# Optimization experiments

Measured on AMD Instinct MI355X. Metric: run time of the kernel, lower is better.

The kernel has to match this reference:

```python
import jax, jax.numpy as jnp
import numpy as np
from jax import lax

B, FREQ, TIME = 32, 256, 4096   # batch, freq bins, time frames
PAD_LEN = 256                   # cfg['n_peaks']
KSIZE = 5                       # cfg['blur_kernel']
SIGMA = 1.0                     # cfg['blur_sigma']


def setup_inputs() -> dict:
    key = jax.random.key(0)
    return {"spec_tensor": jax.random.normal(key, (B, FREQ, TIME), dtype=jnp.float32)}


def _peak_from_features(f):
    # local maxima along time (1x3) and freq (3x1), SAME padding, stride 1
    neg = jnp.asarray(-jnp.inf, f.dtype)
    max_t = lax.reduce_window(f, neg, lax.max, (1, 1, 3), (1, 1, 1), 'SAME')
    max_f = lax.reduce_window(f, neg, lax.max, (1, 3, 1), (1, 1, 1), 'SAME')
    peaks = ((f == max_t) & (f == max_f)).astype(f.dtype)
    mn = jnp.min(f, axis=(1, 2), keepdims=True)
    mx = jnp.max(f, axis=(1, 2), keepdims=True)
    return peaks * ((f - mn) / (mx - mn))


def _gaussian_blur(x):
    # separable gaussian blur with reflect padding (torchvision semantics)
    half = KSIZE // 2
    coords = jnp.arange(KSIZE, dtype=x.dtype) - half
    g = jnp.exp(-0.5 * (coords / SIGMA) ** 2)
    g = g / jnp.sum(g)
    x4 = jnp.pad(x, ((0, 0), (half, half), (half, half)), mode='reflect')[:, None]  # [B,1,F+2h,T+2h]
    kf = g.reshape(1, 1, KSIZE, 1)
    kt = g.reshape(1, 1, 1, KSIZE)
    y = lax.conv_general_dilated(x4, kf, (1, 1), 'VALID')
    y = lax.conv_general_dilated(y, kt, (1, 1), 'VALID')
    return y[:, 0]


def _extract(flat):
    # compact nonzero entries (row-major order) into fixed PAD_LEN slots, zero padded;
    # entries beyond PAD_LEN are truncated (scatter mode='drop').
    mask = flat > 0
    pos = jnp.cumsum(mask.astype(jnp.int32)) - 1
    dest = jnp.where(mask, pos, PAD_LEN)  # out-of-range -> dropped
    idx = jnp.zeros(PAD_LEN, jnp.int32).at[dest].set(
        jnp.arange(flat.shape[0], dtype=jnp.int32), mode='drop')
    val = jnp.zeros(PAD_LEN, flat.dtype).at[dest].set(flat, mode='drop')
    freq = (idx // TIME).astype(flat.dtype) / FREQ
    time = (idx % TIME).astype(flat.dtype) / TIME
    return jnp.stack([freq, time, val], axis=0)  # [3, PAD_LEN]


def reference(spec_tensor):
    p = _peak_from_features(spec_tensor)
    p = _gaussian_blur(p)
    p = _peak_from_features(p)
    return jax.vmap(_extract)(p.reshape(B, FREQ * TIME))  # [B, 3, PAD_LEN]
```

## Files before the change

kernel.cpp:

```cpp
#include <hip/hip_runtime.h>

#define NB 32
#define NF 256
#define NT 4096
#define PAD_LEN 256

#define TF 16
#define TT 128

#define TS 32
#define NSTRIP (NT / TS)

#define G0 0.054488684f
#define G1 0.24420134f
#define G2 0.40261995f

__device__ __forceinline__ float blur5(float a, float b, float c, float d, float e) {
    return G0 * (a + b) + G1 * (c + d) + G2 * e;
}
__device__ __forceinline__ float4 blur5v(const float4& a, const float4& b, const float4& c,
                                         const float4& d, const float4& e) {
    return make_float4(blur5(a.x, b.x, c.x, d.x, e.x), blur5(a.y, b.y, c.y, d.y, e.y),
                       blur5(a.z, b.z, c.z, d.z, e.z), blur5(a.w, b.w, c.w, d.w, e.w));
}

#define SW 140
#define SW4 35
#define RS 24
#define RP 22
#define RV 18

#define R1_WORDS (RS * SW)
#define R2_WORDS (RP * SW)

__device__ __forceinline__ int reflectF(int i) {
    i = (i < 0) ? -i : i;
    return (i >= NF) ? (2 * NF - 2 - i) : i;
}
__device__ __forceinline__ unsigned encf(float x) {
    unsigned u = __float_as_uint(x);
    return (u & 0x80000000u) ? ~u : (u | 0x80000000u);
}
__device__ __forceinline__ float decf(unsigned e) {
    unsigned u = (e & 0x80000000u) ? (e ^ 0x80000000u) : ~e;
    return __uint_as_float(u);
}

#define MM_OFF 0
#define CNT_OFF 1024
#define PFX_OFF (1024 + NB * NF * 32 * 4)

__global__ __launch_bounds__(256) void k_init(float* __restrict__ out, unsigned* __restrict__ mm,
                                              int* __restrict__ counts2) {
    int tid = blockIdx.x * 256 + threadIdx.x;
    if (tid < NB * 3 * PAD_LEN) out[tid] = 0.0f;
    if (tid < NB) {
        mm[tid * 4 + 0] = 0xFFFFFFFFu;
        mm[tid * 4 + 1] = 0u;
        mm[tid * 4 + 2] = 0xFFFFFFFFu;
        mm[tid * 4 + 3] = 0u;
    }
    for (int i = tid; i < NB * NF * 32; i += 96 * 256) counts2[i] = 0;
}

__global__ __launch_bounds__(256) void k_minmax(const float* __restrict__ spec, unsigned* __restrict__ mm) {
    const int b = blockIdx.y;
    const float4* p = (const float4*)(spec + (size_t)b * NF * NT);
    const int base4 = blockIdx.x * 4096;
    float lmin = __builtin_inff(), lmax = -__builtin_inff();
    for (int i = threadIdx.x; i < 4096; i += 256) {
        float4 v = p[base4 + i];
        lmin = fminf(lmin, fminf(fminf(v.x, v.y), fminf(v.z, v.w)));
        lmax = fmaxf(lmax, fmaxf(fmaxf(v.x, v.y), fmaxf(v.z, v.w)));
    }
    for (int off = 32; off; off >>= 1) {
        lmin = fminf(lmin, __shfl_down(lmin, off));
        lmax = fmaxf(lmax, __shfl_down(lmax, off));
    }
    __shared__ float rmn[4], rmx[4];
    int wave = threadIdx.x >> 6, lane = threadIdx.x & 63;
    if (lane == 0) { rmn[wave] = lmin; rmx[wave] = lmax; }
    __syncthreads();
    if (threadIdx.x == 0) {
        for (int w = 1; w < 4; w++) { lmin = fminf(lmin, rmn[w]); lmax = fmaxf(lmax, rmx[w]); }
        atomicMin(&mm[b * 4 + 0], encf(lmin));
        atomicMax(&mm[b * 4 + 1], encf(lmax));
    }
}


template<int J> __device__ __forceinline__ float getj(const float4& v) {
    if constexpr (J == 0) return v.x;
    else if constexpr (J == 1) return v.y;
    else if constexpr (J == 2) return v.z;
    else return v.w;
}

template<bool DP, bool DH, bool DQ, int J>
__device__ __forceinline__ void march_step(
    const float4& r0, const float4& r1, const float4& r2, const float4& r3,
    float4& Sa, float4& Sb, float4& Sc,
    float4& V0, float4& V1, float4& V2, float4& V3, float4& V4,
    float4& Bm, float4& Bc, float4& Bp,
    int& c0, int& c1, int& c2, int& c3,
    float& lmin, float& lmax,
    const int lane, const int sid, const float mn, const float rinv, const int hb)
{
    const float NEGF = -__builtin_inff();
    float4 X = make_float4(getj<J>(r0), getj<J>(r1), getj<J>(r2), getj<J>(r3));
    Sa = Sb; Sb = Sc; Sc = X;
    if constexpr (DP) {
        float up0 = __shfl_up(Sb.w, 1);
        float dn3 = __shfl_down(Sb.x, 1);
        if (lane == 0)  up0 = NEGF;
        if (lane == 63) dn3 = NEGF;
        float4 P;
        { const float x = Sb.x; const bool pk = (x >= Sa.x) && (x >= Sc.x) && (x >= up0)  && (x >= Sb.y); P.x = pk ? (x - mn) * rinv : 0.0f; }
        { const float x = Sb.y; const bool pk = (x >= Sa.y) && (x >= Sc.y) && (x >= Sb.x) && (x >= Sb.z); P.y = pk ? (x - mn) * rinv : 0.0f; }
        { const float x = Sb.z; const bool pk = (x >= Sa.z) && (x >= Sc.z) && (x >= Sb.y) && (x >= Sb.w); P.z = pk ? (x - mn) * rinv : 0.0f; }
        { const float x = Sb.w; const bool pk = (x >= Sa.w) && (x >= Sc.w) && (x >= Sb.z) && (x >= dn3); P.w = pk ? (x - mn) * rinv : 0.0f; }
        const float pzm = __shfl_up(P.z, 1);
        const float pwm = __shfl_up(P.w, 1);
        const float pxp = __shfl_down(P.x, 1);
        const float pyp = __shfl_down(P.y, 1);
        float4 Vn;
        Vn.x = blur5(pzm, P.z, pwm, P.y, P.x);
        Vn.y = blur5(pwm, P.w, P.x, P.z, P.y);
        Vn.z = blur5(P.x, pxp, P.y, P.w, P.z);
        Vn.w = blur5(P.y, pyp, P.z, pxp, P.w);
        if (lane == 0)  { Vn.x = blur5(P.z, P.z, P.y, P.y, P.x);
                          Vn.y = blur5(P.y, P.w, P.x, P.z, P.y); }
        if (lane == 63) { Vn.z = blur5(P.x, P.z, P.y, P.w, P.z);
                          Vn.w = blur5(P.y, P.y, P.z, P.z, P.w); }
        V0 = V1; V1 = V2; V2 = V3; V3 = V4; V4 = Vn;
    }
    if constexpr (DH) {
        const int h = hb + J;
        float4 Bn;
        if ((unsigned)h < (unsigned)NT) {
            Bn = blur5v(V0, V4, V1, V3, V2);
            if (sid == 0) {
                if (h == 0)      Bn = blur5v(V4, V4, V3, V3, V2);
                else if (h == 1) Bn = blur5v(V2, V4, V1, V3, V2);
            }
            if (sid == NSTRIP - 1) {
                if (h == NT - 2)      Bn = blur5v(V0, V2, V1, V3, V2);
                else if (h == NT - 1) Bn = blur5v(V0, V0, V1, V1, V2);
            }
        } else {
            Bn = make_float4(NEGF, NEGF, NEGF, NEGF);
        }
        Bm = Bc; Bc = Bp; Bp = Bn;
    }
    if constexpr (DQ) {
        float u0 = __shfl_up(Bc.w, 1);
        float d3 = __shfl_down(Bc.x, 1);
        if (lane == 0)  u0 = NEGF;
        if (lane == 63) d3 = NEGF;
        { const float x = Bc.x; const bool pk = (x >= Bm.x) && (x >= Bp.x) && (x >= u0)   && (x >= Bc.y); c0 += (pk && (x > 0.0f)) ? 1 : 0; }
        { const float x = Bc.y; const bool pk = (x >= Bm.y) && (x >= Bp.y) && (x >= Bc.x) && (x >= Bc.z); c1 += (pk && (x > 0.0f)) ? 1 : 0; }
        { const float x = Bc.z; const bool pk = (x >= Bm.z) && (x >= Bp.z) && (x >= Bc.y) && (x >= Bc.w); c2 += (pk && (x > 0.0f)) ? 1 : 0; }
        { const float x = Bc.w; const bool pk = (x >= Bm.w) && (x >= Bp.w) && (x >= Bc.z) && (x >= d3); c3 += (pk && (x > 0.0f)) ? 1 : 0; }
        lmin = fminf(lmin, fminf(fminf(Bc.x, Bc.y), fminf(Bc.z, Bc.w)));
        lmax = fmaxf(lmax, fmaxf(fmaxf(Bc.x, Bc.y), fmaxf(Bc.z, Bc.w)));
    }
}

__global__ __launch_bounds__(256) void k_march(const float* __restrict__ spec,
                                               unsigned* __restrict__ mm,
                                               int* __restrict__ counts2) {
    const int b = blockIdx.y;
    const int lane = threadIdx.x & 63;
    const int wv = threadIdx.x >> 6;
    const int sid = blockIdx.x * 4 + wv;
    const int T0 = sid * TS;

    const float mn = decf(mm[b * 4 + 0]);
    const float mx = decf(mm[b * 4 + 1]);
    const float rinv = 1.0f / (mx - mn);

    const float* base = spec + (size_t)b * NF * NT + (size_t)(4 * lane) * NT;
    const float NEGF = -__builtin_inff();
    const float4 NEG4 = make_float4(NEGF, NEGF, NEGF, NEGF);

    float4 a0, a1, a2, a3, b0, b1, b2, b3;
    float4 Sa = NEG4, Sb = NEG4, Sc = NEG4;
    float4 V0 = NEG4, V1 = NEG4, V2 = NEG4, V3 = NEG4, V4 = NEG4;
    float4 Bm = NEG4, Bc = NEG4, Bp = NEG4;
    int c0 = 0, c1 = 0, c2 = 0, c3 = 0;
    float lmin = __builtin_inff(), lmax = NEGF;

#define LOADG(q0, q1, q2, q3, gg) do {                                     \
    const int tg = T0 - 4 + 4 * (gg);                                      \
    if ((unsigned)tg < (unsigned)NT) {                                     \
        q0 = *(const float4*)(base + tg);                                  \
        q1 = *(const float4*)(base + NT + tg);                             \
        q2 = *(const float4*)(base + 2 * NT + tg);                         \
        q3 = *(const float4*)(base + 3 * NT + tg);                         \
    } else { q0 = NEG4; q1 = NEG4; q2 = NEG4; q3 = NEG4; }                 \
} while (0)

#define MARGS Sa, Sb, Sc, V0, V1, V2, V3, V4, Bm, Bc, Bp, c0, c1, c2, c3, lmin, lmax, lane, sid, mn, rinv

    LOADG(a0, a1, a2, a3, 0);
    LOADG(b0, b1, b2, b3, 1);

    march_step<false, false, false, 0>(a0, a1, a2, a3, MARGS, 0);
    march_step<false, false, false, 1>(a0, a1, a2, a3, MARGS, 0);
    march_step<true,  false, false, 2>(a0, a1, a2, a3, MARGS, 0);
    march_step<true,  false, false, 3>(a0, a1, a2, a3, MARGS, 0);
    LOADG(a0, a1, a2, a3, 2);

    {
        const int hb = T0 - 3;
        march_step<true, false, false, 0>(b0, b1, b2, b3, MARGS, hb);
        march_step<true, false, false, 1>(b0, b1, b2, b3, MARGS, hb);
        march_step<true, true,  false, 2>(b0, b1, b2, b3, MARGS, hb);
        march_step<true, true,  false, 3>(b0, b1, b2, b3, MARGS, hb);
    }
    LOADG(b0, b1, b2, b3, 3);

    for (int g = 2; g <= 8; g += 2) {
        {
            const int hb = T0 - 4 + 4 * g - 3;
            march_step<true, true, true, 0>(a0, a1, a2, a3, MARGS, hb);
            march_step<true, true, true, 1>(a0, a1, a2, a3, MARGS, hb);
            march_step<true, true, true, 2>(a0, a1, a2, a3, MARGS, hb);
            march_step<true, true, true, 3>(a0, a1, a2, a3, MARGS, hb);
        }
        if (g + 2 <= 9) LOADG(a0, a1, a2, a3, g + 2);
        {
            const int hb = T0 - 4 + 4 * (g + 1) - 3;
            march_step<true, true, true, 0>(b0, b1, b2, b3, MARGS, hb);
            march_step<true, true, true, 1>(b0, b1, b2, b3, MARGS, hb);
            march_step<true, true, true, 2>(b0, b1, b2, b3, MARGS, hb);
            march_step<true, true, true, 3>(b0, b1, b2, b3, MARGS, hb);
        }
        if (g + 3 <= 9) LOADG(b0, b1, b2, b3, g + 3);
    }

    const int fr = 4 * lane;
    const int cc = sid >> 2;
    atomicAdd(&counts2[(b * NF + fr + 0) * 32 + cc], c0);
    atomicAdd(&counts2[(b * NF + fr + 1) * 32 + cc], c1);
    atomicAdd(&counts2[(b * NF + fr + 2) * 32 + cc], c2);
    atomicAdd(&counts2[(b * NF + fr + 3) * 32 + cc], c3);

    for (int off = 32; off; off >>= 1) {
        lmin = fminf(lmin, __shfl_down(lmin, off));
        lmax = fmaxf(lmax, __shfl_down(lmax, off));
    }
    if (lane == 0) {
        atomicMin(&mm[b * 4 + 2], encf(lmin));
        atomicMax(&mm[b * 4 + 3], encf(lmax));
    }
#undef LOADG
#undef MARGS
}

__device__ __forceinline__ void blur_tile(const float* __restrict__ sb_base,
                                          int f0, int t0, float mn, float rinv,
                                          float* sR1, float* sR2, int tid,
                                          bool f_lo, bool f_hi, bool t_lo, bool t_hi) {
    const float NEG = -__builtin_inff();
    float* sS = sR1;
    float* sV = sR1;
    float* sB = sR2;
    float4* sS4 = (float4*)sR1;
    float4* sP4 = (float4*)sR2;
    float4* sV4 = (float4*)sR1;
    float4* sB4 = (float4*)sR2;

    const bool f_edge = f_lo || f_hi;
    const bool t_edge = t_lo || t_hi;
    const int lane = tid & 63;

    if (!f_edge && !t_edge) {
        const float4* gp = (const float4*)(sb_base + (size_t)(f0 - 4) * NT + (t0 - 4));
        for (int i = tid; i < RS * 34; i += 256) {
            int r = i / 34, c = i - r * 34;
            sS4[r * SW4 + c] = gp[r * (NT / 4) + c];
        }
    } else {
        for (int i = tid; i < RS * 34; i += 256) {
            int r = i / 34, c = i - r * 34;
            int gf = f0 - 4 + r;
            int gc0 = t0 - 4 + 4 * c;
            float4 v = make_float4(NEG, NEG, NEG, NEG);
            if ((unsigned)gf < NF && (unsigned)gc0 < NT)
                v = *(const float4*)(sb_base + (size_t)gf * NT + gc0);
            sS4[r * SW4 + c] = v;
        }
    }
    __syncthreads();

    for (int i = tid; i < RP * 34; i += 256) {
        int r = i / 34, g = i - r * 34;
        const float4 c4 = sS4[(r + 1) * SW4 + g];
        const float4 u4 = sS4[r * SW4 + g];
        const float4 d4 = sS4[(r + 2) * SW4 + g];
        float lm = __shfl_up(c4.w, 1);
        float rp = __shfl_down(c4.x, 1);
        if (lane == 0 && g > 0)   lm = sS[(r + 1) * SW + 4 * g - 1];
        if (lane == 63 && g < 33) rp = sS[(r + 1) * SW + 4 * g + 4];
        float4 o;
        o.x = (c4.x >= lm   && c4.x >= c4.y && c4.x >= u4.x && c4.x >= d4.x) ? (c4.x - mn) * rinv : 0.0f;
        o.y = (c4.y >= c4.x && c4.y >= c4.z && c4.y >= u4.y && c4.y >= d4.y) ? (c4.y - mn) * rinv : 0.0f;
        o.z = (c4.z >= c4.y && c4.z >= c4.w && c4.z >= u4.z && c4.z >= d4.z) ? (c4.z - mn) * rinv : 0.0f;
        o.w = (c4.w >= c4.z && c4.w >= rp   && c4.w >= u4.w && c4.w >= d4.w) ? (c4.w - mn) * rinv : 0.0f;
        if (g == 0) o.x = 0.0f;
        if (g == 33) o.w = 0.0f;
        sP4[r * SW4 + g] = o;
    }
    __syncthreads();

    if (!f_edge) {
        for (int i = tid; i < RV * 34; i += 256) {
            int r = i / 34, g = i - r * 34;
            const float4 p0 = sP4[r * SW4 + g];
            const float4 p1 = sP4[(r + 1) * SW4 + g];
            const float4 p2 = sP4[(r + 2) * SW4 + g];
            const float4 p3 = sP4[(r + 3) * SW4 + g];
            const float4 p4 = sP4[(r + 4) * SW4 + g];
            sV4[r * SW4 + g] = blur5v(p0, p4, p1, p3, p2);
        }
    } else {
        for (int i = tid; i < RV * 34; i += 256) {
            int r = i / 34, g = i - r * 34;
            const int gf = f0 - 1 + r;
            const int r0 = reflectF(gf - 2) - (f0 - 3);
            const int r1 = reflectF(gf - 1) - (f0 - 3);
            const int r2 = gf - (f0 - 3);
            const int r3 = reflectF(gf + 1) - (f0 - 3);
            const int r4 = reflectF(gf + 2) - (f0 - 3);
            const float4 p0 = sP4[r0 * SW4 + g];
            const float4 p1 = sP4[r1 * SW4 + g];
            const float4 p2 = sP4[r2 * SW4 + g];
            const float4 p3 = sP4[r3 * SW4 + g];
            const float4 p4 = sP4[r4 * SW4 + g];
            sV4[r * SW4 + g] = blur5v(p0, p4, p1, p3, p2);
        }
    }
    __syncthreads();

    for (int i = tid; i < RV * 32; i += 256) {
        int r = i >> 5, g = 1 + (i & 31);
        const float4 A = sV4[r * SW4 + g - 1];
        const float4 B = sV4[r * SW4 + g];
        const float4 C = sV4[r * SW4 + g + 1];
        float4 o;
        o.x = blur5(A.z, B.z, A.w, B.y, B.x);
        o.y = blur5(A.w, B.w, B.x, B.z, B.y);
        o.z = blur5(B.x, C.x, B.y, B.w, B.z);
        o.w = blur5(B.y, C.y, B.z, C.x, B.w);
        if (t_lo && g == 1) {
            o.x = blur5(B.z, B.z, B.y, B.y, B.x);
            o.y = blur5(B.y, B.w, B.x, B.z, B.y);
        }
        if (t_hi && g == 32) {
            o.z = blur5(B.x, B.z, B.y, B.w, B.z);
            o.w = blur5(B.y, B.y, B.z, B.z, B.w);
        }
        if ((f_lo && r == 0) || (f_hi && r == 17)) o = make_float4(NEG, NEG, NEG, NEG);
        sB4[r * SW4 + g] = o;
    }
    for (int i = tid; i < RV * 2; i += 256) {
        int r = i >> 1;
        int hi = i & 1;
        int s = hi ? 132 : 3;
        const float* vr = sV + r * SW;
        float v = blur5(vr[s - 2], vr[s + 2], vr[s - 1], vr[s + 1], vr[s]);
        if ((hi ? t_hi : t_lo) || (f_lo && r == 0) || (f_hi && r == 17)) v = NEG;
        sB[r * SW + s] = v;
    }
    __syncthreads();
}

struct Win8 {
    float c[8], l[8], rr[8], u[8], d[8];
};
__device__ __forceinline__ void load_win8(const float4* sB4, int r, int m, Win8& w) {
    const int g = 1 + 2 * m;
    const float4 Cm = sB4[(r + 1) * SW4 + g - 1];
    const float4 C0 = sB4[(r + 1) * SW4 + g];
    const float4 C1 = sB4[(r + 1) * SW4 + g + 1];
    const float4 C2 = sB4[(r + 1) * SW4 + g + 2];
    const float4 U0 = sB4[r * SW4 + g];
    const float4 U1 = sB4[r * SW4 + g + 1];
    const float4 D0 = sB4[(r + 2) * SW4 + g];
    const float4 D1 = sB4[(r + 2) * SW4 + g + 1];
    w.c[0] = C0.x; w.c[1] = C0.y; w.c[2] = C0.z; w.c[3] = C0.w;
    w.c[4] = C1.x; w.c[5] = C1.y; w.c[6] = C1.z; w.c[7] = C1.w;
    w.l[0] = Cm.w; w.l[1] = C0.x; w.l[2] = C0.y; w.l[3] = C0.z;
    w.l[4] = C0.w; w.l[5] = C1.x; w.l[6] = C1.y; w.l[7] = C1.z;
    w.rr[0] = C0.y; w.rr[1] = C0.z; w.rr[2] = C0.w; w.rr[3] = C1.x;
    w.rr[4] = C1.y; w.rr[5] = C1.z; w.rr[6] = C1.w; w.rr[7] = C2.x;
    w.u[0] = U0.x; w.u[1] = U0.y; w.u[2] = U0.z; w.u[3] = U0.w;
    w.u[4] = U1.x; w.u[5] = U1.y; w.u[6] = U1.z; w.u[7] = U1.w;
    w.d[0] = D0.x; w.d[1] = D0.y; w.d[2] = D0.z; w.d[3] = D0.w;
    w.d[4] = D1.x; w.d[5] = D1.y; w.d[6] = D1.z; w.d[7] = D1.w;
}

__global__ __launch_bounds__(256) void k_fallback(const float* __restrict__ spec, unsigned* __restrict__ mm,
                                                  int* __restrict__ counts2) {
    const int b = blockIdx.z;
    const float mn2 = decf(mm[b * 4 + 2]);
    if (mn2 == 0.0f) return;

    const int f0 = blockIdx.y * TF;
    const int t0 = blockIdx.x * TT;
    const int c0 = blockIdx.x;
    const int tid = threadIdx.x;

    __shared__ __align__(16) float sR1[R1_WORDS];
    __shared__ __align__(16) float sR2[R2_WORDS];
    const float4* sB4 = (const float4*)sR2;

    const float mn = decf(mm[b * 4 + 0]);
    const float mx = decf(mm[b * 4 + 1]);
    const float rinv = 1.0f / (mx - mn);
    const float* sb_base = spec + (size_t)b * NF * NT;

    const bool f_lo = (blockIdx.y == 0), f_hi = (blockIdx.y == NF / TF - 1);
    const bool t_lo = (blockIdx.x == 0), t_hi = (blockIdx.x == NT / TT - 1);
    blur_tile(sb_base, f0, t0, mn, rinv, sR1, sR2, tid, f_lo, f_hi, t_lo, t_hi);

    const int r = tid & 15, m = tid >> 4;
    Win8 w;
    load_win8(sB4, r, m, w);
    int cnt = 0;
#pragma unroll
    for (int k = 0; k < 8; k++) {
        float x = w.c[k];
        bool pk = (x >= w.l[k]) && (x >= w.rr[k]) && (x >= w.u[k]) && (x >= w.d[k]);
        cnt += (pk && (x > mn2)) ? 1 : 0;
    }
    __shared__ int pcnt[4][16];
    const int lane = tid & 63, wv = tid >> 6;
    int cs = cnt;
    cs += __shfl_down(cs, 32);
    cs += __shfl_down(cs, 16);
    if (lane < 16) pcnt[wv][lane] = cs;
    __syncthreads();
    if (tid < 16) {
        int tot = pcnt[0][tid] + pcnt[1][tid] + pcnt[2][tid] + pcnt[3][tid];
        counts2[(b * NF + f0 + tid) * 32 + c0] = tot;
    }
}

__global__ __launch_bounds__(256) void k_prefix(const int* __restrict__ counts2, int* __restrict__ prefix2) {
    const int b = blockIdx.x;
    const int tid = threadIdx.x;
    const int* cb = counts2 + b * NF * 32;
    int* pb = prefix2 + b * NF * 32;
    int local[32];
    int s = 0;
    for (int c = 0; c < 32; c++) {
        local[c] = cb[tid * 32 + c];
        s += local[c];
    }
    __shared__ int tot[256];
    tot[tid] = s;
    __syncthreads();
    for (int off = 1; off < 256; off <<= 1) {
        int v = (tid >= off) ? tot[tid - off] : 0;
        __syncthreads();
        tot[tid] += v;
        __syncthreads();
    }
    int run = tot[tid] - s;
    for (int c = 0; c < 32; c++) {
        pb[tid * 32 + c] = run;
        run += local[c];
    }
}

__global__ __launch_bounds__(256) void k_extract(const float* __restrict__ spec, unsigned* __restrict__ mm,
                                                 const int* __restrict__ prefix2, float* __restrict__ out) {
    const int b = blockIdx.z;
    const int f0 = blockIdx.y * TF;
    const int t0 = blockIdx.x * TT;
    const int c0 = blockIdx.x;
    if (prefix2[(b * NF + f0) * 32 + c0] >= PAD_LEN) return;

    const int tid = threadIdx.x;
    __shared__ __align__(16) float sR1[R1_WORDS];
    __shared__ __align__(16) float sR2[R2_WORDS];
    const float4* sB4 = (const float4*)sR2;

    const float mn = decf(mm[b * 4 + 0]);
    const float mx = decf(mm[b * 4 + 1]);
    const float rinv = 1.0f / (mx - mn);
    const float mn2 = decf(mm[b * 4 + 2]);
    const float mx2 = decf(mm[b * 4 + 3]);
    const float rinv2 = 1.0f / (mx2 - mn2);
    const float* sb_base = spec + (size_t)b * NF * NT;

    const bool f_lo = (blockIdx.y == 0), f_hi = (blockIdx.y == NF / TF - 1);
    const bool t_lo = (blockIdx.x == 0), t_hi = (blockIdx.x == NT / TT - 1);
    blur_tile(sb_base, f0, t0, mn, rinv, sR1, sR2, tid, f_lo, f_hi, t_lo, t_hi);

    const int r = tid & 15, m = tid >> 4;
    const int gf = f0 + r;
    const int base = prefix2[(b * NF + gf) * 32 + c0];
    Win8 w;
    load_win8(sB4, r, m, w);
    bool pos[8];
    int mycnt = 0;
#pragma unroll
    for (int k = 0; k < 8; k++) {
        float x = w.c[k];
        pos[k] = (x >= w.l[k]) && (x >= w.rr[k]) && (x >= w.u[k]) && (x >= w.d[k]) && (x > mn2);
        mycnt += pos[k] ? 1 : 0;
    }
    const int lane = tid & 63, wv = tid >> 6, p = (tid >> 4) & 3;
    int s = mycnt;
    int t1 = __shfl_up(s, 16); if (p >= 1) s += t1;
    int t2 = __shfl_up(s, 32); if (p >= 2) s += t2;
    __shared__ int wtot[4][16];
    if (p == 3) wtot[wv][lane & 15] = s;
    __syncthreads();
    int woff = 0;
    for (int w2 = 0; w2 < wv; ++w2) woff += wtot[w2][r];
    int rank = base + woff + (s - mycnt);
#pragma unroll
    for (int k = 0; k < 8; k++) {
        if (pos[k]) {
            if (rank < PAD_LEN) {
                int gc = t0 + 8 * m + k;
                out[b * 768 + rank]       = (float)gf * (1.0f / 256.0f);
                out[b * 768 + 256 + rank] = (float)gc * (1.0f / 4096.0f);
                out[b * 768 + 512 + rank] = (w.c[k] - mn2) * rinv2;
            }
            rank++;
        }
    }
}

extern "C" void kernel_launch(void* const* d_in, const int* in_sizes, int n_in,
                              void* d_out, int out_size, void* d_ws, size_t ws_size,
                              hipStream_t stream) {
    const float* spec = (const float*)d_in[0];
    float* out = (float*)d_out;
    unsigned* mm = (unsigned*)((char*)d_ws + MM_OFF);
    int* counts2 = (int*)((char*)d_ws + CNT_OFF);
    int* prefix2 = (int*)((char*)d_ws + PFX_OFF);

    k_init<<<96, 256, 0, stream>>>(out, mm, counts2);
    k_minmax<<<dim3(64, NB), 256, 0, stream>>>(spec, mm);
    k_march<<<dim3(NSTRIP / 4, NB), 256, 0, stream>>>(spec, mm, counts2);
    dim3 tgrid(NT / TT, NF / TF, NB);
    k_fallback<<<tgrid, 256, 0, stream>>>(spec, mm, counts2);
    k_prefix<<<NB, 256, 0, stream>>>(counts2, prefix2);
    k_extract<<<tgrid, 256, 0, stream>>>(spec, mm, prefix2, out);
}
```

Baseline: 404.2 us.

## Stage march kernel global loads through LDS for coalesced row reads

```diff
diff --git a/kernel.cpp b/kernel.cpp
--- a/kernel.cpp
+++ b/kernel.cpp
@@ -32,6 +32,8 @@
 
 #define R1_WORDS (RS * SW)
 #define R2_WORDS (RP * SW)
+
+#define MPAD 12
 
 __device__ __forceinline__ int reflectF(int i) {
     i = (i < 0) ? -i : i;
@@ -179,65 +181,95 @@
     const float mx = decf(mm[b * 4 + 1]);
     const float rinv = 1.0f / (mx - mn);
 
-    const float* base = spec + (size_t)b * NF * NT + (size_t)(4 * lane) * NT;
     const float NEGF = -__builtin_inff();
     const float4 NEG4 = make_float4(NEGF, NEGF, NEGF, NEGF);
 
-    float4 a0, a1, a2, a3, b0, b1, b2, b3;
+    __shared__ __align__(16) float sStage[4][256 * MPAD];
+    float* myS = sStage[wv];
+
+    const int srow = lane >> 1;
+    const int shalf = lane & 1;
+    const float* gsrc = spec + (size_t)b * NF * NT + (size_t)srow * NT + 4 * shalf;
+
+    float4 R[8];
+    float4 A[4];
+
+#define GLOAD(G) do {                                                          \
+    const int tg = T0 - 4 + 8 * (G);                                           \
+    const bool ok = (unsigned)(tg + 4 * shalf) < (unsigned)NT;                 \
+    _Pragma("unroll")                                                          \
+    for (int i = 0; i < 8; ++i)                                                \
+        R[i] = ok ? *(const float4*)(gsrc + (size_t)(32 * i) * NT + tg) : NEG4; \
+} while (0)
+
+#define SWRITE() do {                                                          \
+    _Pragma("unroll")                                                          \
+    for (int i = 0; i < 8; ++i)                                                \
+        *(float4*)(myS + (32 * i + srow) * MPAD + 4 * shalf) = R[i];           \
+} while (0)
+
+#define SREAD(c) do {                                                          \
+    _Pragma("unroll")                                                          \
+    for (int j = 0; j < 4; ++j)                                                \
+        A[j] = *(const float4*)(myS + (4 * lane + j) * MPAD + (c));            \
+} while (0)
+
     float4 Sa = NEG4, Sb = NEG4, Sc = NEG4;
     float4 V0 = NEG4, V1 = NEG4, V2 = NEG4, V3 = NEG4, V4 = NEG4;
     float4 Bm = NEG4, Bc = NEG4, Bp = NEG4;
     int c0 = 0, c1 = 0, c2 = 0, c3 = 0;
     float lmin = __builtin_inff(), lmax = NEGF;
 
-#define LOADG(q0, q1, q2, q3, gg) do {                                     \
-    const int tg = T0 - 4 + 4 * (gg);                                      \
-    if ((unsigned)tg < (unsigned)NT) {                                     \
-        q0 = *(const float4*)(base + tg);                                  \
-        q1 = *(const float4*)(base + NT + tg);                             \
-        q2 = *(const float4*)(base + 2 * NT + tg);                         \
-        q3 = *(const float4*)(base + 3 * NT + tg);                         \
-    } else { q0 = NEG4; q1 = NEG4; q2 = NEG4; q3 = NEG4; }                 \
-} while (0)
-
 #define MARGS Sa, Sb, Sc, V0, V1, V2, V3, V4, Bm, Bc, Bp, c0, c1, c2, c3, lmin, lmax, lane, sid, mn, rinv
 
-    LOADG(a0, a1, a2, a3, 0);
-    LOADG(b0, b1, b2, b3, 1);
-
-    march_step<false, false, false, 0>(a0, a1, a2, a3, MARGS, 0);
-    march_step<false, false, false, 1>(a0, a1, a2, a3, MARGS, 0);
-    march_step<true,  false, false, 2>(a0, a1, a2, a3, MARGS, 0);
-    march_step<true,  false, false, 3>(a0, a1, a2, a3, MARGS, 0);
-    LOADG(a0, a1, a2, a3, 2);
-
+    GLOAD(0);
+    SWRITE();
+    GLOAD(1);
+    SREAD(0);
+    march_step<false, false, false, 0>(A[0], A[1], A[2], A[3], MARGS, 0);
+    march_step<false, false, false, 1>(A[0], A[1], A[2], A[3], MARGS, 0);
+    march_step<true,  false, false, 2>(A[0], A[1], A[2], A[3], MARGS, 0);
+    march_step<true,  false, false, 3>(A[0], A[1], A[2], A[3], MARGS, 0);
+    SREAD(4);
     {
         const int hb = T0 - 3;
-        march_step<true, false, false, 0>(b0, b1, b2, b3, MARGS, hb);
-        march_step<true, false, false, 1>(b0, b1, b2, b3, MARGS, hb);
-        march_step<true, true,  false, 2>(b0, b1, b2, b3, MARGS, hb);
-        march_step<true, true,  false, 3>(b0, b1, b2, b3, MARGS, hb);
-    }
-    LOADG(b0, b1, b2, b3, 3);
-
-    for (int g = 2; g <= 8; g += 2) {
-        {
-            const int hb = T0 - 4 + 4 * g - 3;
-            march_step<true, true, true, 0>(a0, a1, a2, a3, MARGS, hb);
-            march_step<true, true, true, 1>(a0, a1, a2, a3, MARGS, hb);
-            march_step<true, true, true, 2>(a0, a1, a2, a3, MARGS, hb);
-            march_step<true, true, true, 3>(a0, a1, a2, a3, MARGS, hb);
-        }
-        if (g + 2 <= 9) LOADG(a0, a1, a2, a3, g + 2);
-        {
-            const int hb = T0 - 4 + 4 * (g + 1) - 3;
-            march_step<true, true, true, 0>(b0, b1, b2, b3, MARGS, hb);
-            march_step<true, true, true, 1>(b0, b1, b2, b3, MARGS, hb);
-            march_step<true, true, true, 2>(b0, b1, b2, b3, MARGS, hb);
-            march_step<true, true, true, 3>(b0, b1, b2, b3, MARGS, hb);
-        }
-        if (g + 3 <= 9) LOADG(b0, b1, b2, b3, g + 3);
-    }
+        march_step<true, false, false, 0>(A[0], A[1], A[2], A[3], MARGS, hb);
+        march_step<true, false, false, 1>(A[0], A[1], A[2], A[3], MARGS, hb);
+        march_step<true, true,  false, 2>(A[0], A[1], A[2], A[3], MARGS, hb);
+        march_step<true, true,  false, 3>(A[0], A[1], A[2], A[3], MARGS, hb);
+    }
+
+#define STEADY_GROUP(G) do {                                                   \
+    SWRITE();                                                                  \
+    if ((G) < 4) GLOAD((G) + 1);                                               \
+    SREAD(0);                                                                  \
+    {                                                                          \
+        const int hb = T0 + 8 * (G) - 7;           \
+        march_step<true, true, true, 0>(A[0], A[1], A[2], A[3], MARGS, hb);    \
+        march_step<true, true, true, 1>(A[0], A[1], A[2], A[3], MARGS, hb);    \
+        march_step<true, true, true, 2>(A[0], A[1], A[2], A[3], MARGS, hb);    \
+        march_step<true, true, true, 3>(A[0], A[1], A[2], A[3], MARGS, hb);    \
+    }                                                                          \
+    SREAD(4);                                                                  \
+    {                                                                          \
+        const int hb = T0 + 8 * (G) - 3;                         \
+        march_step<true, true, true, 0>(A[0], A[1], A[2], A[3], MARGS, hb);    \
+        march_step<true, true, true, 1>(A[0], A[1], A[2], A[3], MARGS, hb);    \
+        march_step<true, true, true, 2>(A[0], A[1], A[2], A[3], MARGS, hb);    \
+        march_step<true, true, true, 3>(A[0], A[1], A[2], A[3], MARGS, hb);    \
+    }                                                                          \
+} while (0)
+
+    STEADY_GROUP(1);
+    STEADY_GROUP(2);
+    STEADY_GROUP(3);
+    STEADY_GROUP(4);
+
+#undef STEADY_GROUP
+#undef GLOAD
+#undef SWRITE
+#undef SREAD
+#undef MARGS
 
     const int fr = 4 * lane;
     const int cc = sid >> 2;
@@ -254,8 +286,6 @@
         atomicMin(&mm[b * 4 + 2], encf(lmin));
         atomicMax(&mm[b * 4 + 3], encf(lmax));
     }
-#undef LOADG
-#undef MARGS
 }
 
 __device__ __forceinline__ void blur_tile(const float* __restrict__ sb_base,
```

Measured after the change: 382.0 us. 1.06x faster.
